# Kernel tuning notes

Hardware: AMD Instinct MI355X
Metric: run time of the kernel (lower is better)

Reference implementation:

```python
import jax, jax.numpy as jnp
import numpy as np

N, T, D = 32768, 2048, 2
CLAMP_SIGMA2_MIN = 1e-12


def setup_inputs() -> dict:
    key = jax.random.key(0)
    z = jax.random.normal(key, (N, T, D), dtype=jnp.float32)
    # per-dimension GARCH(1,1) parameters (stationary: alpha + beta < 1)
    omega = 0.05 * jnp.ones((D,), jnp.float32)
    alpha = 0.08 * jnp.ones((D,), jnp.float32)
    beta = 0.90 * jnp.ones((D,), jnp.float32)
    mu = jnp.zeros((D,), jnp.float32)
    sigma2_0 = jnp.ones((D,), jnp.float32)
    return {"z": z, "omega": omega, "alpha": alpha, "beta": beta,
            "mu": mu, "sigma2_0": sigma2_0}


def reference(z, omega, alpha, beta, mu, sigma2_0):
    # z: (N, T, d) iid noise; params: (d,). GARCH(1,1) per dimension:
    #   sigma_t^2 = omega + alpha * eps_{t-1}^2 + beta * sigma_{t-1}^2
    #   eps_t = sigma_t * z_t ;  x_t = mu + eps_t
    n, t, d = z.shape

    def step(carry, z_t):
        eps2_prev, sig2_prev = carry            # each (N, d)
        sig2 = omega + alpha * eps2_prev + beta * sig2_prev
        sig2 = jnp.maximum(sig2, CLAMP_SIGMA2_MIN)
        eps = jnp.sqrt(sig2) * z_t
        return (eps * eps, sig2), mu + eps

    eps2_init = jnp.zeros((n, d), z.dtype)
    sig2_init = jnp.broadcast_to(sigma2_0.astype(z.dtype), (n, d))
    _, x_tnd = jax.lax.scan(step, (eps2_init, sig2_init), jnp.swapaxes(z, 0, 1))
    return jnp.swapaxes(x_tnd, 0, 1)            # (N, T, d)
```

## Files before the change

kernel.cpp:

```cpp
#include <hip/hip_runtime.h>
#include <hip/hip_bf16.h>


#define GARCH_N 32768
#define GARCH_T 2048
#define GARCH_D 2
#define F4_PER_CHAIN (GARCH_T * GARCH_D / 4)
#define CHUNK 8

__global__ __launch_bounds__(128) void garch_kernel(
    const float4* __restrict__ z4,
    const float* __restrict__ omega,
    const float* __restrict__ alpha,
    const float* __restrict__ beta,
    const float* __restrict__ mu,
    const float* __restrict__ sigma2_0,
    float4* __restrict__ x4)
{
    const int n = blockIdx.x * blockDim.x + threadIdx.x;
    if (n >= GARCH_N) return;

    const float o0 = omega[0], o1 = omega[1];
    const float a0 = alpha[0], a1 = alpha[1];
    const float b0 = beta[0],  b1 = beta[1];
    const float m0 = mu[0],    m1 = mu[1];

    float s2a = sigma2_0[0], s2b = sigma2_0[1];
    float e2a = 0.0f,        e2b = 0.0f;

    const float4* __restrict__ zp = z4 + (size_t)n * F4_PER_CHAIN;
    float4* __restrict__ xp       = x4 + (size_t)n * F4_PER_CHAIN;

    for (int c = 0; c < F4_PER_CHAIN; c += CHUNK) {
        float4 in[CHUNK];
        #pragma unroll
        for (int j = 0; j < CHUNK; ++j) in[j] = zp[c + j];

        float4 out[CHUNK];
        #pragma unroll
        for (int j = 0; j < CHUNK; ++j) {
            const float4 v = in[j];
            s2a = fmaf(b0, s2a, fmaf(a0, e2a, o0));
            s2a = fmaxf(s2a, 1e-12f);
            float ea = sqrtf(s2a) * v.x;
            float xa = m0 + ea;
            e2a = ea * ea;

            s2b = fmaf(b1, s2b, fmaf(a1, e2b, o1));
            s2b = fmaxf(s2b, 1e-12f);
            float eb = sqrtf(s2b) * v.y;
            float xb = m1 + eb;
            e2b = eb * eb;

            s2a = fmaf(b0, s2a, fmaf(a0, e2a, o0));
            s2a = fmaxf(s2a, 1e-12f);
            float ec = sqrtf(s2a) * v.z;
            float xc = m0 + ec;
            e2a = ec * ec;

            s2b = fmaf(b1, s2b, fmaf(a1, e2b, o1));
            s2b = fmaxf(s2b, 1e-12f);
            float ed = sqrtf(s2b) * v.w;
            float xd = m1 + ed;
            e2b = ed * ed;

            out[j] = make_float4(xa, xb, xc, xd);
        }

        #pragma unroll
        for (int j = 0; j < CHUNK; ++j) xp[c + j] = out[j];
    }
}

extern "C" void kernel_launch(void* const* d_in, const int* in_sizes, int n_in,
                              void* d_out, int out_size, void* d_ws, size_t ws_size,
                              hipStream_t stream)
{
    const float4* z4      = (const float4*)d_in[0];
    const float* omega    = (const float*)d_in[1];
    const float* alpha    = (const float*)d_in[2];
    const float* beta     = (const float*)d_in[3];
    const float* mu       = (const float*)d_in[4];
    const float* sigma2_0 = (const float*)d_in[5];
    float4* x4            = (float4*)d_out;

    const int block = 128;
    const int grid  = (GARCH_N + block - 1) / block;
    garch_kernel<<<grid, block, 0, stream>>>(z4, omega, alpha, beta, mu, sigma2_0, x4);
}
```

Baseline: 1.040 ms.

## Double-buffer z loads across chunks to overlap memory with the recurrence

Adds two register buffers of 16 float4 each, so the next chunk of z is prefetched while the current chunk runs the serial GARCH recurrence. Output stores are now issued inside the compute loop rather than batched at the end. The chunk size doubles from 8 to 16. This is meant to hide global load latency behind the dependent sqrt/fma chain, at the cost of more registers per thread, which may reduce occupancy.

```diff
diff --git a/kernel.cpp b/kernel.cpp
--- a/kernel.cpp
+++ b/kernel.cpp
@@ -4,9 +4,50 @@
 
 #define GARCH_N 32768
 #define GARCH_T 2048
-#define GARCH_D 2
-#define F4_PER_CHAIN (GARCH_T * GARCH_D / 4)
-#define CHUNK 8
+#define F4_PER_CHAIN (GARCH_T * 2 / 4)
+#define CHUNK 16
+#define NCHUNK (F4_PER_CHAIN / CHUNK)
+
+struct GarchState {
+    float s2a, s2b, e2a, e2b;
+    float o0, o1, a0, a1, b0, b1, m0, m1;
+};
+
+__device__ __forceinline__ void garch_chunk(const float4 (&in)[CHUNK],
+                                            float4* __restrict__ xp, int c,
+                                            GarchState& st)
+{
+    #pragma unroll
+    for (int j = 0; j < CHUNK; ++j) {
+        const float4 v = in[j];
+
+        st.s2a = fmaf(st.b0, st.s2a, fmaf(st.a0, st.e2a, st.o0));
+        st.s2a = fmaxf(st.s2a, 1e-12f);
+        float ea = sqrtf(st.s2a) * v.x;
+        float xa = st.m0 + ea;
+        st.e2a = ea * ea;
+
+        st.s2b = fmaf(st.b1, st.s2b, fmaf(st.a1, st.e2b, st.o1));
+        st.s2b = fmaxf(st.s2b, 1e-12f);
+        float eb = sqrtf(st.s2b) * v.y;
+        float xb = st.m1 + eb;
+        st.e2b = eb * eb;
+
+        st.s2a = fmaf(st.b0, st.s2a, fmaf(st.a0, st.e2a, st.o0));
+        st.s2a = fmaxf(st.s2a, 1e-12f);
+        float ec = sqrtf(st.s2a) * v.z;
+        float xc = st.m0 + ec;
+        st.e2a = ec * ec;
+
+        st.s2b = fmaf(st.b1, st.s2b, fmaf(st.a1, st.e2b, st.o1));
+        st.s2b = fmaxf(st.s2b, 1e-12f);
+        float ed = sqrtf(st.s2b) * v.w;
+        float xd = st.m1 + ed;
+        st.e2b = ed * ed;
+
+        xp[c + j] = make_float4(xa, xb, xc, xd);
+    }
+}
 
 __global__ __launch_bounds__(128) void garch_kernel(
     const float4* __restrict__ z4,
@@ -20,55 +61,34 @@
     const int n = blockIdx.x * blockDim.x + threadIdx.x;
     if (n >= GARCH_N) return;
 
-    const float o0 = omega[0], o1 = omega[1];
-    const float a0 = alpha[0], a1 = alpha[1];
-    const float b0 = beta[0],  b1 = beta[1];
-    const float m0 = mu[0],    m1 = mu[1];
-
-    float s2a = sigma2_0[0], s2b = sigma2_0[1];
-    float e2a = 0.0f,        e2b = 0.0f;
+    GarchState st;
+    st.o0 = omega[0]; st.o1 = omega[1];
+    st.a0 = alpha[0]; st.a1 = alpha[1];
+    st.b0 = beta[0];  st.b1 = beta[1];
+    st.m0 = mu[0];    st.m1 = mu[1];
+    st.s2a = sigma2_0[0]; st.s2b = sigma2_0[1];
+    st.e2a = 0.0f;        st.e2b = 0.0f;
 
     const float4* __restrict__ zp = z4 + (size_t)n * F4_PER_CHAIN;
     float4* __restrict__ xp       = x4 + (size_t)n * F4_PER_CHAIN;
 
-    for (int c = 0; c < F4_PER_CHAIN; c += CHUNK) {
-        float4 in[CHUNK];
+    float4 bufA[CHUNK], bufB[CHUNK];
+
+    #pragma unroll
+    for (int j = 0; j < CHUNK; ++j) bufA[j] = zp[j];
+
+    for (int c = 0; c < NCHUNK; c += 2) {
         #pragma unroll
-        for (int j = 0; j < CHUNK; ++j) in[j] = zp[c + j];
+        for (int j = 0; j < CHUNK; ++j) bufB[j] = zp[(c + 1) * CHUNK + j];
 
-        float4 out[CHUNK];
-        #pragma unroll
-        for (int j = 0; j < CHUNK; ++j) {
-            const float4 v = in[j];
-            s2a = fmaf(b0, s2a, fmaf(a0, e2a, o0));
-            s2a = fmaxf(s2a, 1e-12f);
-            float ea = sqrtf(s2a) * v.x;
-            float xa = m0 + ea;
-            e2a = ea * ea;
+        garch_chunk(bufA, xp, c * CHUNK, st);
 
-            s2b = fmaf(b1, s2b, fmaf(a1, e2b, o1));
-            s2b = fmaxf(s2b, 1e-12f);
-            float eb = sqrtf(s2b) * v.y;
-            float xb = m1 + eb;
-            e2b = eb * eb;
-
-            s2a = fmaf(b0, s2a, fmaf(a0, e2a, o0));
-            s2a = fmaxf(s2a, 1e-12f);
-            float ec = sqrtf(s2a) * v.z;
-            float xc = m0 + ec;
-            e2a = ec * ec;
-
-            s2b = fmaf(b1, s2b, fmaf(a1, e2b, o1));
-            s2b = fmaxf(s2b, 1e-12f);
-            float ed = sqrtf(s2b) * v.w;
-            float xd = m1 + ed;
-            e2b = ed * ed;
-
-            out[j] = make_float4(xa, xb, xc, xd);
+        if (c + 2 < NCHUNK) {
+            #pragma unroll
+            for (int j = 0; j < CHUNK; ++j) bufA[j] = zp[(c + 2) * CHUNK + j];
         }
 
-        #pragma unroll
-        for (int j = 0; j < CHUNK; ++j) xp[c + j] = out[j];
+        garch_chunk(bufB, xp, (c + 1) * CHUNK, st);
     }
 }
 
```

Measured after the change: 992.7 us. 1.05x faster.
